# Optimization experiments

Hardware: AMD Instinct MI355X
Metric: run time of the kernel (lower is better)

## Reference

```python
import jax, jax.numpy as jnp
import numpy as np

KSIZE = 3  # median window

def median_blur(x, k):
    # x: [B, C, H, W]; zero padding (k-1)//2, median over k*k window
    # (matches kornia's conv2d-with-binary-kernels + median implementation)
    p = (k - 1) // 2
    xp = jnp.pad(x, ((0, 0), (0, 0), (p, p), (p, p)))
    B, C, H, W = x.shape
    # stack k*k shifted views -> [B, C, H, W, k*k] (k*k=9, small static loop)
    patches = jnp.stack(
        [xp[:, :, i:i + H, j:j + W] for i in range(k) for j in range(k)],
        axis=-1,
    )
    return jnp.median(patches, axis=-1)


def setup_inputs() -> dict:
    key = jax.random.key(0)
    k1, k2, k3 = jax.random.split(key, 3)
    B, C, H, W = 32, 256, 64, 64
    x = jax.random.normal(k1, (B, C, H, W), dtype=jnp.float32)
    # 1x1 conv weight [out_c, in_c] (the trailing 1x1 spatial dims are squeezed)
    conv_w = jax.random.normal(k2, (C, C), dtype=jnp.float32) * (1.0 / np.sqrt(C))
    conv_b = jax.random.normal(k3, (C,), dtype=jnp.float32) * 0.01
    return {"x": x, "conv_w": conv_w, "conv_b": conv_b}


def reference(x, conv_w, conv_b):
    x_denoised = median_blur(x, KSIZE)  # [B, C, H, W]
    # 1x1 conv == per-pixel channel mixing GEMM
    conv_out = jnp.einsum("oc,bchw->bohw", conv_w, x_denoised) + conv_b[None, :, None, None]
    return x + conv_out
```

## Files before the change

kernel.cpp:

```cpp
#include <hip/hip_runtime.h>

typedef float f32x4 __attribute__((ext_vector_type(4)));
typedef __bf16 bf16x8 __attribute__((ext_vector_type(8)));
typedef unsigned short u16x8 __attribute__((ext_vector_type(8)));

__device__ __forceinline__ unsigned short f2bf(float f) {
  union { float f; unsigned u; } v; v.f = f;
  unsigned r = v.u + 0x7FFFu + ((v.u >> 16) & 1u);
  return (unsigned short)(r >> 16);
}

__device__ __forceinline__ float min3f(float a, float b, float c) {
  return fminf(fminf(a, b), c);
}
__device__ __forceinline__ float max3f(float a, float b, float c) {
  return fmaxf(fmaxf(a, b), c);
}
__device__ __forceinline__ float med3f(float a, float b, float c) {
  return __builtin_amdgcn_fmed3f(a, b, c);
}

__device__ __forceinline__ void gload_lds16(const void* g, void* l) {
  __builtin_amdgcn_global_load_lds(
      (const __attribute__((address_space(1))) void*)g,
      (__attribute__((address_space(3))) void*)l, 16, 0, 0);
}

__global__ void wconv_k(const float* __restrict__ w, unsigned short* __restrict__ wbf) {
  int idx  = blockIdx.x * 256 + threadIdx.x;
  int lane = idx & 63;
  int ob   = (idx >> 6) & 15;
  int ks   = idx >> 10;
  int o = (ob << 4) + (lane & 15);
  int c = (ks << 5) + ((lane >> 4) << 3);
  const float* src = w + (o << 8) + c;
  f32x4 v0 = *(const f32x4*)src;
  f32x4 v1 = *(const f32x4*)(src + 4);
  u16x8 ov;
  ov[0] = f2bf(v0[0]); ov[1] = f2bf(v0[1]); ov[2] = f2bf(v0[2]); ov[3] = f2bf(v0[3]);
  ov[4] = f2bf(v1[0]); ov[5] = f2bf(v1[1]); ov[6] = f2bf(v1[2]); ov[7] = f2bf(v1[3]);
  *(u16x8*)(wbf + (idx << 3)) = ov;
}

__launch_bounds__(256, 2)
__global__ void fused_k(const float* __restrict__ x,
                        const unsigned short* __restrict__ wbf,
                        const float* __restrict__ bias,
                        float* __restrict__ out) {
  __shared__ float Xs[128][64];
  __shared__ unsigned short Bt[128][40];

  const int t   = threadIdx.x;
  const int blk = blockIdx.x;
  const int swz = ((blk & 7) << 7) | (blk >> 3);
  const int b   = swz >> 5;
  const int r0  = (swz & 31) << 1;
  const int lane = t & 63;
  const int w    = t >> 6;
  const int g    = lane >> 4;
  const int l15  = lane & 15;

  const int ci  = t >> 3;
  const int s   = t & 7;
  const int px0 = s << 3;
  const int cw  = ci ^ ((s & 3) << 3);
  const bool hasL = (s > 0), hasR = (s < 7);
  const bool zTop = (r0 == 0), zBot = (r0 == 62);

  const float* xb = x + ((size_t)b << 20);

  float bn[4];
  #pragma unroll
  for (int n = 0; n < 4; ++n) bn[n] = bias[(w << 6) + (n << 4) + l15];

  unsigned soff[8];
  #pragma unroll
  for (int p = 0; p < 8; ++p) {
    int cp = (w << 3) + p;
    int gr = r0 + (lane >> 4) - 1;
    gr = gr < 0 ? 0 : (gr > 63 ? 63 : gr);
    int bG = (lane & 15) ^ p;
    soff[p] = ((unsigned)cp << 14) + ((unsigned)gr << 8) + ((unsigned)bG << 4);
  }

  auto stage = [&](int step) {
    const unsigned kso = (unsigned)step << 19;
    #pragma unroll
    for (int p = 0; p < 8; ++p)
      gload_lds16((const char*)xb + (soff[p] + kso), &Xs[(w << 5) + (p << 2)][0]);
  };

  f32x4 acc[8][4];
  #pragma unroll
  for (int m = 0; m < 8; ++m)
    #pragma unroll
    for (int n = 0; n < 4; ++n)
      acc[m][n] = (f32x4){0.f, 0.f, 0.f, 0.f};

  stage(0);
  __syncthreads();

  const int ri0 = ci << 2;
  const int sig = ci & 7;
  const int bA  = ((s << 1)) ^ sig;
  const int bB  = ((s << 1) | 1) ^ sig;

  #pragma unroll
  for (int ks = 0; ks < 8; ++ks) {
    bf16x8 wfc[4];
    #pragma unroll
    for (int n = 0; n < 4; ++n) {
      const int fidx = (((ks << 4) + (w << 2) + n) << 6) + lane;
      wfc[n] = __builtin_bit_cast(bf16x8, *(const u16x8*)(wbf + ((size_t)fidx << 3)));
    }

    f32x4 va[4], vb[4];
    #pragma unroll
    for (int dr = 0; dr < 4; ++dr) {
      const float* rp = &Xs[ri0 + dr][0];
      va[dr] = *(const f32x4*)(rp + (bA << 2));
      vb[dr] = *(const f32x4*)(rp + (bB << 2));
    }
    float le[4], re[4];
    #pragma unroll
    for (int dr = 0; dr < 4; ++dr) {
      le[dr] = __shfl_up(vb[dr][3], 1);
      re[dr] = __shfl_down(va[dr][0], 1);
    }

    if ((ks >> 1) == w) {
      const int h = ks & 1;
      #pragma unroll
      for (int nn = 0; nn < 2; ++nn) {
        const int n  = (h << 1) + nn;
        const int cx = (nn << 4) + l15;
        const int sx = cx & 7;
        const int rb = cx << 2;
        #pragma unroll
        for (int m = 0; m < 8; ++m) {
          const int bL = ((((m & 3) << 2) + g) ^ sx) << 2;
          const f32x4 xv = *(const f32x4*)&Xs[rb + 1 + (m >> 2)][bL];
          acc[m][n] += xv;
        }
      }
    }

    {
      float R0[10], R1[10], R2[10];
      R0[0] = hasL ? le[0] : 0.f; R1[0] = hasL ? le[1] : 0.f; R2[0] = hasL ? le[2] : 0.f;
      R0[9] = hasR ? re[0] : 0.f; R1[9] = hasR ? re[1] : 0.f; R2[9] = hasR ? re[2] : 0.f;
      #pragma unroll
      for (int j = 0; j < 4; ++j) {
        R0[1 + j] = va[0][j]; R0[5 + j] = vb[0][j];
        R1[1 + j] = va[1][j]; R1[5 + j] = vb[1][j];
        R2[1 + j] = va[2][j]; R2[5 + j] = vb[2][j];
      }
      if (zTop) {
        #pragma unroll
        for (int j = 0; j < 10; ++j) R0[j] = 0.f;
      }
      float mn[10], md[10], mx[10];
      #pragma unroll
      for (int j = 0; j < 10; ++j) {
        mn[j] = min3f(R0[j], R1[j], R2[j]);
        md[j] = med3f(R0[j], R1[j], R2[j]);
        mx[j] = max3f(R0[j], R1[j], R2[j]);
      }
      #pragma unroll
      for (int i = 0; i < 8; ++i) {
        float t0 = max3f(mn[i], mn[i+1], mn[i+2]);
        float t1 = med3f(md[i], md[i+1], md[i+2]);
        float t2 = min3f(mx[i], mx[i+1], mx[i+2]);
        Bt[px0 + i][cw] = f2bf(med3f(t0, t1, t2));
      }
    }
    {
      float R0[10], R1[10], R2[10];
      R0[0] = hasL ? le[1] : 0.f; R1[0] = hasL ? le[2] : 0.f; R2[0] = hasL ? le[3] : 0.f;
      R0[9] = hasR ? re[1] : 0.f; R1[9] = hasR ? re[2] : 0.f; R2[9] = hasR ? re[3] : 0.f;
      #pragma unroll
      for (int j = 0; j < 4; ++j) {
        R0[1 + j] = va[1][j]; R0[5 + j] = vb[1][j];
        R1[1 + j] = va[2][j]; R1[5 + j] = vb[2][j];
        R2[1 + j] = va[3][j]; R2[5 + j] = vb[3][j];
      }
      if (zBot) {
        #pragma unroll
        for (int j = 0; j < 10; ++j) R2[j] = 0.f;
      }
      float mn[10], md[10], mx[10];
      #pragma unroll
      for (int j = 0; j < 10; ++j) {
        mn[j] = min3f(R0[j], R1[j], R2[j]);
        md[j] = med3f(R0[j], R1[j], R2[j]);
        mx[j] = max3f(R0[j], R1[j], R2[j]);
      }
      #pragma unroll
      for (int i = 0; i < 8; ++i) {
        float t0 = max3f(mn[i], mn[i+1], mn[i+2]);
        float t1 = med3f(md[i], md[i+1], md[i+2]);
        float t2 = min3f(mx[i], mx[i+1], mx[i+2]);
        Bt[64 + px0 + i][cw] = f2bf(med3f(t0, t1, t2));
      }
    }

    __syncthreads();

    if (ks < 7) stage(ks + 1);

    bf16x8 pa[8];
    #pragma unroll
    for (int m = 0; m < 8; ++m) {
      const int px = (m << 4) + l15;
      const int gc = (g ^ ((px >> 3) & 3)) << 3;
      pa[m] = __builtin_bit_cast(bf16x8, *(const u16x8*)&Bt[px][gc]);
    }
    #pragma unroll
    for (int m = 0; m < 8; ++m)
      #pragma unroll
      for (int n = 0; n < 4; ++n)
        acc[m][n] = __builtin_amdgcn_mfma_f32_16x16x32_bf16(pa[m], wfc[n], acc[m][n], 0, 0, 0);

    if (ks < 7) __syncthreads();
  }

  #pragma unroll
  for (int m = 0; m < 8; ++m) {
    #pragma unroll
    for (int n = 0; n < 4; ++n) {
      const int o = (w << 6) + (n << 4) + l15;
      const size_t idx = ((((size_t)b << 8) + (size_t)o) << 12)
                       + ((size_t)(r0 + (m >> 2)) << 6)
                       + (size_t)(((m & 3) << 4) + (g << 2));
      f32x4 res;
      #pragma unroll
      for (int q = 0; q < 4; ++q) res[q] = acc[m][n][q] + bn[n];
      *(f32x4*)(out + idx) = res;
    }
  }
}

extern "C" void kernel_launch(void* const* d_in, const int* in_sizes, int n_in,
                              void* d_out, int out_size, void* d_ws, size_t ws_size,
                              hipStream_t stream) {
  const float* x  = (const float*)d_in[0];
  const float* cw = (const float*)d_in[1];
  const float* cb = (const float*)d_in[2];
  float* out = (float*)d_out;
  unsigned short* wbf = (unsigned short*)d_ws;

  hipLaunchKernelGGL(wconv_k, dim3(32), dim3(256), 0, stream, cw, wbf);
  hipLaunchKernelGGL(fused_k, dim3(1024), dim3(256), 0, stream, x, wbf, cb, out);
}
```

Baseline: 65.59 us.

## Stage input tile as bf16 in LDS via register prefetch instead of direct LDS loads

The input tile is now loaded into registers, converted to bf16, and written to LDS with a new swizzle, replacing the fp32 direct global-to-LDS loads. This halves LDS footprint and read traffic, and lets the next tile's global loads overlap the MFMA phase. The median and residual now run on bf16-rounded inputs, so the residual term loses precision against the fp32 reference. Output stores also become nontemporal.

```diff
diff --git a/kernel.cpp b/kernel.cpp
--- a/kernel.cpp
+++ b/kernel.cpp
@@ -3,13 +3,28 @@
 typedef float f32x4 __attribute__((ext_vector_type(4)));
 typedef __bf16 bf16x8 __attribute__((ext_vector_type(8)));
 typedef unsigned short u16x8 __attribute__((ext_vector_type(8)));
+typedef unsigned short u16x4 __attribute__((ext_vector_type(4)));
 
 __device__ __forceinline__ unsigned short f2bf(float f) {
   union { float f; unsigned u; } v; v.f = f;
   unsigned r = v.u + 0x7FFFu + ((v.u >> 16) & 1u);
   return (unsigned short)(r >> 16);
 }
-
+__device__ __forceinline__ float bf2f(unsigned short u) {
+  union { unsigned u; float f; } v; v.u = (unsigned)u << 16; return v.f;
+}
+__device__ __forceinline__ unsigned short f2bf_exact(float f) {
+  union { float f; unsigned u; } v; v.f = f;
+  return (unsigned short)(v.u >> 16);
+}
+__device__ __forceinline__ u16x4 cvt4(f32x4 v) {
+  u16x4 o;
+  o[0] = __builtin_bit_cast(unsigned short, (__bf16)v[0]);
+  o[1] = __builtin_bit_cast(unsigned short, (__bf16)v[1]);
+  o[2] = __builtin_bit_cast(unsigned short, (__bf16)v[2]);
+  o[3] = __builtin_bit_cast(unsigned short, (__bf16)v[3]);
+  return o;
+}
 __device__ __forceinline__ float min3f(float a, float b, float c) {
   return fminf(fminf(a, b), c);
 }
@@ -18,12 +33,6 @@
 }
 __device__ __forceinline__ float med3f(float a, float b, float c) {
   return __builtin_amdgcn_fmed3f(a, b, c);
-}
-
-__device__ __forceinline__ void gload_lds16(const void* g, void* l) {
-  __builtin_amdgcn_global_load_lds(
-      (const __attribute__((address_space(1))) void*)g,
-      (__attribute__((address_space(3))) void*)l, 16, 0, 0);
 }
 
 __global__ void wconv_k(const float* __restrict__ w, unsigned short* __restrict__ wbf) {
@@ -47,7 +56,7 @@
                         const unsigned short* __restrict__ wbf,
                         const float* __restrict__ bias,
                         float* __restrict__ out) {
-  __shared__ float Xs[128][64];
+  __shared__ unsigned short Xs[128][64];
   __shared__ unsigned short Bt[128][40];
 
   const int t   = threadIdx.x;
@@ -73,21 +82,31 @@
   #pragma unroll
   for (int n = 0; n < 4; ++n) bn[n] = bias[(w << 6) + (n << 4) + l15];
 
-  unsigned soff[8];
+  const int dr_st = lane >> 4;
+  const int g16   = lane & 15;
+  unsigned soff[8], wdst[8];
   #pragma unroll
   for (int p = 0; p < 8; ++p) {
     int cp = (w << 3) + p;
-    int gr = r0 + (lane >> 4) - 1;
+    int gr = r0 + dr_st - 1;
     gr = gr < 0 ? 0 : (gr > 63 ? 63 : gr);
-    int bG = (lane & 15) ^ p;
-    soff[p] = ((unsigned)cp << 14) + ((unsigned)gr << 8) + ((unsigned)bG << 4);
+    soff[p] = ((unsigned)cp << 14) + ((unsigned)gr << 8) + ((unsigned)g16 << 4);
+    int gs = (g16 >> 1) ^ p ^ dr_st;
+    wdst[p] = (unsigned)(((cp << 2) + dr_st) << 6) + (unsigned)(gs << 3) + (unsigned)((g16 & 1) << 2);
   }
-
-  auto stage = [&](int step) {
+  unsigned short* XsF = &Xs[0][0];
+
+  f32x4 ld[8];
+  auto issue = [&](int step) {
     const unsigned kso = (unsigned)step << 19;
     #pragma unroll
     for (int p = 0; p < 8; ++p)
-      gload_lds16((const char*)xb + (soff[p] + kso), &Xs[(w << 5) + (p << 2)][0]);
+      ld[p] = *(const f32x4*)((const char*)xb + (soff[p] + kso));
+  };
+  auto commit = [&]() {
+    #pragma unroll
+    for (int p = 0; p < 8; ++p)
+      *(u16x4*)&XsF[wdst[p]] = cvt4(ld[p]);
   };
 
   f32x4 acc[8][4];
@@ -97,13 +116,8 @@
     for (int n = 0; n < 4; ++n)
       acc[m][n] = (f32x4){0.f, 0.f, 0.f, 0.f};
 
-  stage(0);
+  issue(0); commit();
   __syncthreads();
-
-  const int ri0 = ci << 2;
-  const int sig = ci & 7;
-  const int bA  = ((s << 1)) ^ sig;
-  const int bB  = ((s << 1) | 1) ^ sig;
 
   #pragma unroll
   for (int ks = 0; ks < 8; ++ks) {
@@ -114,18 +128,11 @@
       wfc[n] = __builtin_bit_cast(bf16x8, *(const u16x8*)(wbf + ((size_t)fidx << 3)));
     }
 
-    f32x4 va[4], vb[4];
+    u16x8 xv[4];
     #pragma unroll
     for (int dr = 0; dr < 4; ++dr) {
-      const float* rp = &Xs[ri0 + dr][0];
-      va[dr] = *(const f32x4*)(rp + (bA << 2));
-      vb[dr] = *(const f32x4*)(rp + (bB << 2));
-    }
-    float le[4], re[4];
-    #pragma unroll
-    for (int dr = 0; dr < 4; ++dr) {
-      le[dr] = __shfl_up(vb[dr][3], 1);
-      re[dr] = __shfl_down(va[dr][0], 1);
+      const int gs = s ^ (ci & 7) ^ dr;
+      xv[dr] = *(const u16x8*)&XsF[(((ci << 2) + dr) << 6) + (gs << 3)];
     }
 
     if ((ks >> 1) == w) {
@@ -134,15 +141,28 @@
       for (int nn = 0; nn < 2; ++nn) {
         const int n  = (h << 1) + nn;
         const int cx = (nn << 4) + l15;
-        const int sx = cx & 7;
-        const int rb = cx << 2;
         #pragma unroll
         for (int m = 0; m < 8; ++m) {
-          const int bL = ((((m & 3) << 2) + g) ^ sx) << 2;
-          const f32x4 xv = *(const f32x4*)&Xs[rb + 1 + (m >> 2)][bL];
-          acc[m][n] += xv;
+          const int dr = 1 + (m >> 2);
+          const int gf = ((m & 3) << 1) + (g >> 1);
+          const int gs = gf ^ (cx & 7) ^ dr;
+          const u16x4 xv4 = *(const u16x4*)&XsF[(((cx << 2) + dr) << 6) + (gs << 3) + ((g & 1) << 2)];
+          #pragma unroll
+          for (int q = 0; q < 4; ++q) acc[m][n][q] += bf2f(xv4[q]);
         }
       }
+    }
+
+    float X[4][8];
+    #pragma unroll
+    for (int dr = 0; dr < 4; ++dr)
+      #pragma unroll
+      for (int j = 0; j < 8; ++j) X[dr][j] = bf2f(xv[dr][j]);
+    float le[4], re[4];
+    #pragma unroll
+    for (int dr = 0; dr < 4; ++dr) {
+      le[dr] = __shfl_up(X[dr][7], 1);
+      re[dr] = __shfl_down(X[dr][0], 1);
     }
 
     {
@@ -150,11 +170,7 @@
       R0[0] = hasL ? le[0] : 0.f; R1[0] = hasL ? le[1] : 0.f; R2[0] = hasL ? le[2] : 0.f;
       R0[9] = hasR ? re[0] : 0.f; R1[9] = hasR ? re[1] : 0.f; R2[9] = hasR ? re[2] : 0.f;
       #pragma unroll
-      for (int j = 0; j < 4; ++j) {
-        R0[1 + j] = va[0][j]; R0[5 + j] = vb[0][j];
-        R1[1 + j] = va[1][j]; R1[5 + j] = vb[1][j];
-        R2[1 + j] = va[2][j]; R2[5 + j] = vb[2][j];
-      }
+      for (int j = 0; j < 8; ++j) { R0[1 + j] = X[0][j]; R1[1 + j] = X[1][j]; R2[1 + j] = X[2][j]; }
       if (zTop) {
         #pragma unroll
         for (int j = 0; j < 10; ++j) R0[j] = 0.f;
@@ -171,7 +187,7 @@
         float t0 = max3f(mn[i], mn[i+1], mn[i+2]);
         float t1 = med3f(md[i], md[i+1], md[i+2]);
         float t2 = min3f(mx[i], mx[i+1], mx[i+2]);
-        Bt[px0 + i][cw] = f2bf(med3f(t0, t1, t2));
+        Bt[px0 + i][cw] = f2bf_exact(med3f(t0, t1, t2));
       }
     }
     {
@@ -179,11 +195,7 @@
       R0[0] = hasL ? le[1] : 0.f; R1[0] = hasL ? le[2] : 0.f; R2[0] = hasL ? le[3] : 0.f;
       R0[9] = hasR ? re[1] : 0.f; R1[9] = hasR ? re[2] : 0.f; R2[9] = hasR ? re[3] : 0.f;
       #pragma unroll
-      for (int j = 0; j < 4; ++j) {
-        R0[1 + j] = va[1][j]; R0[5 + j] = vb[1][j];
-        R1[1 + j] = va[2][j]; R1[5 + j] = vb[2][j];
-        R2[1 + j] = va[3][j]; R2[5 + j] = vb[3][j];
-      }
+      for (int j = 0; j < 8; ++j) { R0[1 + j] = X[1][j]; R1[1 + j] = X[2][j]; R2[1 + j] = X[3][j]; }
       if (zBot) {
         #pragma unroll
         for (int j = 0; j < 10; ++j) R2[j] = 0.f;
@@ -200,13 +212,14 @@
         float t0 = max3f(mn[i], mn[i+1], mn[i+2]);
         float t1 = med3f(md[i], md[i+1], md[i+2]);
         float t2 = min3f(mx[i], mx[i+1], mx[i+2]);
-        Bt[64 + px0 + i][cw] = f2bf(med3f(t0, t1, t2));
+        Bt[64 + px0 + i][cw] = f2bf_exact(med3f(t0, t1, t2));
       }
     }
 
     __syncthreads();
 
-    if (ks < 7) stage(ks + 1);
+    if (ks < 7) issue(ks + 1);
+    __builtin_amdgcn_sched_barrier(0);
 
     bf16x8 pa[8];
     #pragma unroll
@@ -221,7 +234,9 @@
       for (int n = 0; n < 4; ++n)
         acc[m][n] = __builtin_amdgcn_mfma_f32_16x16x32_bf16(pa[m], wfc[n], acc[m][n], 0, 0, 0);
 
-    if (ks < 7) __syncthreads();
+    if (ks < 7) commit();
+
+    __syncthreads();
   }
 
   #pragma unroll
@@ -235,7 +250,7 @@
       f32x4 res;
       #pragma unroll
       for (int q = 0; q < 4; ++q) res[q] = acc[m][n][q] + bn[n];
-      *(f32x4*)(out + idx) = res;
+      __builtin_nontemporal_store(res, (f32x4*)(out + idx));
     }
   }
 }
```

Measured after the change: 97.84 us. 1.49x slower.

## Double-buffer x tiles in LDS with manual waitcnt and barrier scheduling

Applied to the files above, without the earlier changes.

Splits the LDS input tile into two buffers and prefetches the x slab two K-steps ahead, replacing __syncthreads with explicit s_waitcnt/s_barrier and sched_barrier fences. MFMA issue gets raised priority with s_setprio. The residual add moves from per-iteration LDS reads into the epilogue as a global read of x. The aim is to hide global-to-LDS latency behind the median and MFMA work and to drop LDS traffic from the loop. The cost is extra LDS, an extra global read of x, and fragile hand-placed waits: cross-wave visibility and buffer reuse now depend on counter waits rather than full barriers.

```diff
diff --git a/kernel.cpp b/kernel.cpp
--- a/kernel.cpp
+++ b/kernel.cpp
@@ -9,7 +9,6 @@
   unsigned r = v.u + 0x7FFFu + ((v.u >> 16) & 1u);
   return (unsigned short)(r >> 16);
 }
-
 __device__ __forceinline__ float min3f(float a, float b, float c) {
   return fminf(fminf(a, b), c);
 }
@@ -47,7 +46,7 @@
                         const unsigned short* __restrict__ wbf,
                         const float* __restrict__ bias,
                         float* __restrict__ out) {
-  __shared__ float Xs[128][64];
+  __shared__ float Xs[2][128][64];
   __shared__ unsigned short Bt[128][40];
 
   const int t   = threadIdx.x;
@@ -83,11 +82,11 @@
     soff[p] = ((unsigned)cp << 14) + ((unsigned)gr << 8) + ((unsigned)bG << 4);
   }
 
-  auto stage = [&](int step) {
+  auto stage = [&](int step, int buf) {
     const unsigned kso = (unsigned)step << 19;
     #pragma unroll
     for (int p = 0; p < 8; ++p)
-      gload_lds16((const char*)xb + (soff[p] + kso), &Xs[(w << 5) + (p << 2)][0]);
+      gload_lds16((const char*)xb + (soff[p] + kso), &Xs[buf][(w << 5) + (p << 2)][0]);
   };
 
   f32x4 acc[8][4];
@@ -97,8 +96,8 @@
     for (int n = 0; n < 4; ++n)
       acc[m][n] = (f32x4){0.f, 0.f, 0.f, 0.f};
 
-  stage(0);
-  __syncthreads();
+  stage(0, 0);
+  stage(1, 1);
 
   const int ri0 = ci << 2;
   const int sig = ci & 7;
@@ -107,106 +106,98 @@
 
   #pragma unroll
   for (int ks = 0; ks < 8; ++ks) {
+    asm volatile("s_waitcnt vmcnt(8)" ::: "memory");
+    __builtin_amdgcn_sched_barrier(0);
+
+    f32x4 va[4], vb[4];
+    #pragma unroll
+    for (int dr = 0; dr < 4; ++dr) {
+      const float* rp = &Xs[ks & 1][ri0 + dr][0];
+      va[dr] = *(const f32x4*)(rp + (bA << 2));
+      vb[dr] = *(const f32x4*)(rp + (bB << 2));
+    }
+    asm volatile("s_waitcnt lgkmcnt(0)" ::: "memory");
+    __builtin_amdgcn_sched_barrier(0);
+
     bf16x8 wfc[4];
     #pragma unroll
     for (int n = 0; n < 4; ++n) {
       const int fidx = (((ks << 4) + (w << 2) + n) << 6) + lane;
       wfc[n] = __builtin_bit_cast(bf16x8, *(const u16x8*)(wbf + ((size_t)fidx << 3)));
     }
-
-    f32x4 va[4], vb[4];
-    #pragma unroll
-    for (int dr = 0; dr < 4; ++dr) {
-      const float* rp = &Xs[ri0 + dr][0];
-      va[dr] = *(const f32x4*)(rp + (bA << 2));
-      vb[dr] = *(const f32x4*)(rp + (bB << 2));
-    }
-    float le[4], re[4];
-    #pragma unroll
-    for (int dr = 0; dr < 4; ++dr) {
-      le[dr] = __shfl_up(vb[dr][3], 1);
-      re[dr] = __shfl_down(va[dr][0], 1);
-    }
-
-    if ((ks >> 1) == w) {
-      const int h = ks & 1;
+    __builtin_amdgcn_sched_barrier(0);
+    if (ks < 6) stage(ks + 2, ks & 1);
+    __builtin_amdgcn_sched_barrier(0);
+
+    {
+      float le[4], re[4];
       #pragma unroll
-      for (int nn = 0; nn < 2; ++nn) {
-        const int n  = (h << 1) + nn;
-        const int cx = (nn << 4) + l15;
-        const int sx = cx & 7;
-        const int rb = cx << 2;
-        #pragma unroll
-        for (int m = 0; m < 8; ++m) {
-          const int bL = ((((m & 3) << 2) + g) ^ sx) << 2;
-          const f32x4 xv = *(const f32x4*)&Xs[rb + 1 + (m >> 2)][bL];
-          acc[m][n] += xv;
-        }
+      for (int dr = 0; dr < 4; ++dr) {
+        le[dr] = __shfl_up(vb[dr][3], 1);
+        re[dr] = __shfl_down(va[dr][0], 1);
       }
-    }
-
-    {
-      float R0[10], R1[10], R2[10];
-      R0[0] = hasL ? le[0] : 0.f; R1[0] = hasL ? le[1] : 0.f; R2[0] = hasL ? le[2] : 0.f;
-      R0[9] = hasR ? re[0] : 0.f; R1[9] = hasR ? re[1] : 0.f; R2[9] = hasR ? re[2] : 0.f;
-      #pragma unroll
-      for (int j = 0; j < 4; ++j) {
-        R0[1 + j] = va[0][j]; R0[5 + j] = vb[0][j];
-        R1[1 + j] = va[1][j]; R1[5 + j] = vb[1][j];
-        R2[1 + j] = va[2][j]; R2[5 + j] = vb[2][j];
+      {
+        float R0[10], R1[10], R2[10];
+        R0[0] = hasL ? le[0] : 0.f; R1[0] = hasL ? le[1] : 0.f; R2[0] = hasL ? le[2] : 0.f;
+        R0[9] = hasR ? re[0] : 0.f; R1[9] = hasR ? re[1] : 0.f; R2[9] = hasR ? re[2] : 0.f;
+        #pragma unroll
+        for (int j = 0; j < 4; ++j) {
+          R0[1 + j] = va[0][j]; R0[5 + j] = vb[0][j];
+          R1[1 + j] = va[1][j]; R1[5 + j] = vb[1][j];
+          R2[1 + j] = va[2][j]; R2[5 + j] = vb[2][j];
+        }
+        if (zTop) {
+          #pragma unroll
+          for (int j = 0; j < 10; ++j) R0[j] = 0.f;
+        }
+        float mn[10], md[10], mx[10];
+        #pragma unroll
+        for (int j = 0; j < 10; ++j) {
+          mn[j] = min3f(R0[j], R1[j], R2[j]);
+          md[j] = med3f(R0[j], R1[j], R2[j]);
+          mx[j] = max3f(R0[j], R1[j], R2[j]);
+        }
+        #pragma unroll
+        for (int i = 0; i < 8; ++i) {
+          float t0 = max3f(mn[i], mn[i+1], mn[i+2]);
+          float t1 = med3f(md[i], md[i+1], md[i+2]);
+          float t2 = min3f(mx[i], mx[i+1], mx[i+2]);
+          Bt[px0 + i][cw] = f2bf(med3f(t0, t1, t2));
+        }
       }
-      if (zTop) {
-        #pragma unroll
-        for (int j = 0; j < 10; ++j) R0[j] = 0.f;
+      {
+        float R0[10], R1[10], R2[10];
+        R0[0] = hasL ? le[1] : 0.f; R1[0] = hasL ? le[2] : 0.f; R2[0] = hasL ? le[3] : 0.f;
+        R0[9] = hasR ? re[1] : 0.f; R1[9] = hasR ? re[2] : 0.f; R2[9] = hasR ? re[3] : 0.f;
+        #pragma unroll
+        for (int j = 0; j < 4; ++j) {
+          R0[1 + j] = va[1][j]; R0[5 + j] = vb[1][j];
+          R1[1 + j] = va[2][j]; R1[5 + j] = vb[2][j];
+          R2[1 + j] = va[3][j]; R2[5 + j] = vb[3][j];
+        }
+        if (zBot) {
+          #pragma unroll
+          for (int j = 0; j < 10; ++j) R2[j] = 0.f;
+        }
+        float mn[10], md[10], mx[10];
+        #pragma unroll
+        for (int j = 0; j < 10; ++j) {
+          mn[j] = min3f(R0[j], R1[j], R2[j]);
+          md[j] = med3f(R0[j], R1[j], R2[j]);
+          mx[j] = max3f(R0[j], R1[j], R2[j]);
+        }
+        #pragma unroll
+        for (int i = 0; i < 8; ++i) {
+          float t0 = max3f(mn[i], mn[i+1], mn[i+2]);
+          float t1 = med3f(md[i], md[i+1], md[i+2]);
+          float t2 = min3f(mx[i], mx[i+1], mx[i+2]);
+          Bt[64 + px0 + i][cw] = f2bf(med3f(t0, t1, t2));
+        }
       }
-      float mn[10], md[10], mx[10];
-      #pragma unroll
-      for (int j = 0; j < 10; ++j) {
-        mn[j] = min3f(R0[j], R1[j], R2[j]);
-        md[j] = med3f(R0[j], R1[j], R2[j]);
-        mx[j] = max3f(R0[j], R1[j], R2[j]);
-      }
-      #pragma unroll
-      for (int i = 0; i < 8; ++i) {
-        float t0 = max3f(mn[i], mn[i+1], mn[i+2]);
-        float t1 = med3f(md[i], md[i+1], md[i+2]);
-        float t2 = min3f(mx[i], mx[i+1], mx[i+2]);
-        Bt[px0 + i][cw] = f2bf(med3f(t0, t1, t2));
-      }
-    }
-    {
-      float R0[10], R1[10], R2[10];
-      R0[0] = hasL ? le[1] : 0.f; R1[0] = hasL ? le[2] : 0.f; R2[0] = hasL ? le[3] : 0.f;
-      R0[9] = hasR ? re[1] : 0.f; R1[9] = hasR ? re[2] : 0.f; R2[9] = hasR ? re[3] : 0.f;
-      #pragma unroll
-      for (int j = 0; j < 4; ++j) {
-        R0[1 + j] = va[1][j]; R0[5 + j] = vb[1][j];
-        R1[1 + j] = va[2][j]; R1[5 + j] = vb[2][j];
-        R2[1 + j] = va[3][j]; R2[5 + j] = vb[3][j];
-      }
-      if (zBot) {
-        #pragma unroll
-        for (int j = 0; j < 10; ++j) R2[j] = 0.f;
-      }
-      float mn[10], md[10], mx[10];
-      #pragma unroll
-      for (int j = 0; j < 10; ++j) {
-        mn[j] = min3f(R0[j], R1[j], R2[j]);
-        md[j] = med3f(R0[j], R1[j], R2[j]);
-        mx[j] = max3f(R0[j], R1[j], R2[j]);
-      }
-      #pragma unroll
-      for (int i = 0; i < 8; ++i) {
-        float t0 = max3f(mn[i], mn[i+1], mn[i+2]);
-        float t1 = med3f(md[i], md[i+1], md[i+2]);
-        float t2 = min3f(mx[i], mx[i+1], mx[i+2]);
-        Bt[64 + px0 + i][cw] = f2bf(med3f(t0, t1, t2));
-      }
-    }
-
-    __syncthreads();
-
-    if (ks < 7) stage(ks + 1);
+    }
+
+    asm volatile("s_waitcnt lgkmcnt(0)\n\ts_barrier" ::: "memory");
+    __builtin_amdgcn_sched_barrier(0);
 
     bf16x8 pa[8];
     #pragma unroll
@@ -215,13 +206,17 @@
       const int gc = (g ^ ((px >> 3) & 3)) << 3;
       pa[m] = __builtin_bit_cast(bf16x8, *(const u16x8*)&Bt[px][gc]);
     }
+
+    __builtin_amdgcn_s_setprio(1);
     #pragma unroll
     for (int m = 0; m < 8; ++m)
       #pragma unroll
       for (int n = 0; n < 4; ++n)
         acc[m][n] = __builtin_amdgcn_mfma_f32_16x16x32_bf16(pa[m], wfc[n], acc[m][n], 0, 0, 0);
-
-    if (ks < 7) __syncthreads();
+    __builtin_amdgcn_s_setprio(0);
+
+    asm volatile("s_barrier" ::: "memory");
+    __builtin_amdgcn_sched_barrier(0);
   }
 
   #pragma unroll
@@ -232,9 +227,10 @@
       const size_t idx = ((((size_t)b << 8) + (size_t)o) << 12)
                        + ((size_t)(r0 + (m >> 2)) << 6)
                        + (size_t)(((m & 3) << 4) + (g << 2));
+      f32x4 xv = *(const f32x4*)(x + idx);
       f32x4 res;
       #pragma unroll
-      for (int q = 0; q < 4; ++q) res[q] = acc[m][n][q] + bn[n];
+      for (int q = 0; q < 4; ++q) res[q] = xv[q] + acc[m][n][q] + bn[n];
       *(f32x4*)(out + idx) = res;
     }
   }
```

New measurement: 78.56 us. 1.2x slower.

## Double threads per block to 512 and halve per-thread median and MFMA work

Applied to the files above, without the earlier changes.

Launches the fused median+GEMM kernel with 512 threads (8 waves) instead of 256. Each wave now owns 32 output channels instead of 64, and each thread computes medians for 4 pixels instead of 8. Staging, LDS swizzles and residual loads are remapped to match. The goal is lower register pressure and more waves in flight to hide LDS and global latency, at the cost of more shuffles per output and less reuse of each loaded A fragment across MFMAs.

```diff
diff --git a/kernel.cpp b/kernel.cpp
--- a/kernel.cpp
+++ b/kernel.cpp
@@ -42,7 +42,7 @@
   *(u16x8*)(wbf + (idx << 3)) = ov;
 }
 
-__launch_bounds__(256, 2)
+__launch_bounds__(512, 4)
 __global__ void fused_k(const float* __restrict__ x,
                         const unsigned short* __restrict__ wbf,
                         const float* __restrict__ bias,
@@ -60,147 +60,118 @@
   const int g    = lane >> 4;
   const int l15  = lane & 15;
 
-  const int ci  = t >> 3;
-  const int s   = t & 7;
-  const int px0 = s << 3;
-  const int cw  = ci ^ ((s & 3) << 3);
-  const bool hasL = (s > 0), hasR = (s < 7);
+  const int ci  = t >> 4;
+  const int s   = lane & 15;
+  const int px0 = s << 2;
+  const int cw  = ci ^ (((s >> 1) & 3) << 3);
+  const bool hasL = (s > 0), hasR = (s < 15);
   const bool zTop = (r0 == 0), zBot = (r0 == 62);
 
   const float* xb = x + ((size_t)b << 20);
 
-  float bn[4];
-  #pragma unroll
-  for (int n = 0; n < 4; ++n) bn[n] = bias[(w << 6) + (n << 4) + l15];
-
-  unsigned soff[8];
-  #pragma unroll
-  for (int p = 0; p < 8; ++p) {
-    int cp = (w << 3) + p;
+  float bn[2];
+  #pragma unroll
+  for (int n = 0; n < 2; ++n) bn[n] = bias[(w << 5) + (n << 4) + l15];
+
+  unsigned soff[4];
+  #pragma unroll
+  for (int p = 0; p < 4; ++p) {
+    int cp = (w << 2) + p;
     int gr = r0 + (lane >> 4) - 1;
     gr = gr < 0 ? 0 : (gr > 63 ? 63 : gr);
-    int bG = (lane & 15) ^ p;
-    soff[p] = ((unsigned)cp << 14) + ((unsigned)gr << 8) + ((unsigned)bG << 4);
+    int gG = (lane & 15) ^ (cp & 3);
+    soff[p] = ((unsigned)cp << 14) + ((unsigned)gr << 8) + ((unsigned)gG << 4);
   }
 
   auto stage = [&](int step) {
     const unsigned kso = (unsigned)step << 19;
     #pragma unroll
-    for (int p = 0; p < 8; ++p)
-      gload_lds16((const char*)xb + (soff[p] + kso), &Xs[(w << 5) + (p << 2)][0]);
+    for (int p = 0; p < 4; ++p)
+      gload_lds16((const char*)xb + (soff[p] + kso), &Xs[((w << 2) + p) << 2][0]);
   };
 
-  f32x4 acc[8][4];
+  f32x4 acc[8][2];
   #pragma unroll
   for (int m = 0; m < 8; ++m)
     #pragma unroll
-    for (int n = 0; n < 4; ++n)
+    for (int n = 0; n < 2; ++n)
       acc[m][n] = (f32x4){0.f, 0.f, 0.f, 0.f};
 
   stage(0);
   __syncthreads();
 
   const int ri0 = ci << 2;
-  const int sig = ci & 7;
-  const int bA  = ((s << 1)) ^ sig;
-  const int bB  = ((s << 1) | 1) ^ sig;
+  const int gsw = s ^ (ci & 3);
 
   #pragma unroll
   for (int ks = 0; ks < 8; ++ks) {
-    bf16x8 wfc[4];
-    #pragma unroll
-    for (int n = 0; n < 4; ++n) {
-      const int fidx = (((ks << 4) + (w << 2) + n) << 6) + lane;
+    bf16x8 wfc[2];
+    #pragma unroll
+    for (int n = 0; n < 2; ++n) {
+      const int fidx = (((ks << 4) + (w << 1) + n) << 6) + lane;
       wfc[n] = __builtin_bit_cast(bf16x8, *(const u16x8*)(wbf + ((size_t)fidx << 3)));
     }
 
-    f32x4 va[4], vb[4];
+    f32x4 va[4];
+    #pragma unroll
+    for (int dr = 0; dr < 4; ++dr)
+      va[dr] = *(const f32x4*)&Xs[ri0 + dr][gsw << 2];
+    float le[4], re[4];
     #pragma unroll
     for (int dr = 0; dr < 4; ++dr) {
-      const float* rp = &Xs[ri0 + dr][0];
-      va[dr] = *(const f32x4*)(rp + (bA << 2));
-      vb[dr] = *(const f32x4*)(rp + (bB << 2));
-    }
-    float le[4], re[4];
-    #pragma unroll
-    for (int dr = 0; dr < 4; ++dr) {
-      le[dr] = __shfl_up(vb[dr][3], 1);
+      le[dr] = __shfl_up(va[dr][3], 1);
       re[dr] = __shfl_down(va[dr][0], 1);
     }
 
-    if ((ks >> 1) == w) {
-      const int h = ks & 1;
-      #pragma unroll
-      for (int nn = 0; nn < 2; ++nn) {
-        const int n  = (h << 1) + nn;
-        const int cx = (nn << 4) + l15;
-        const int sx = cx & 7;
-        const int rb = cx << 2;
+    if (ks == w) {
+      #pragma unroll
+      for (int n = 0; n < 2; ++n) {
+        const int cx = (n << 4) + l15;
         #pragma unroll
         for (int m = 0; m < 8; ++m) {
-          const int bL = ((((m & 3) << 2) + g) ^ sx) << 2;
-          const f32x4 xv = *(const f32x4*)&Xs[rb + 1 + (m >> 2)][bL];
+          const int dr = 1 + (m >> 2);
+          const int gf = ((m & 3) << 2) + g;
+          const int gs = gf ^ (cx & 3);
+          const f32x4 xv = *(const f32x4*)&Xs[(cx << 2) + dr][gs << 2];
           acc[m][n] += xv;
         }
       }
     }
 
-    {
-      float R0[10], R1[10], R2[10];
-      R0[0] = hasL ? le[0] : 0.f; R1[0] = hasL ? le[1] : 0.f; R2[0] = hasL ? le[2] : 0.f;
-      R0[9] = hasR ? re[0] : 0.f; R1[9] = hasR ? re[1] : 0.f; R2[9] = hasR ? re[2] : 0.f;
+    #pragma unroll
+    for (int strip = 0; strip < 2; ++strip) {
+      const int d0 = strip;
+      float R0[6], R1[6], R2[6];
+      R0[0] = hasL ? le[d0]     : 0.f;  R0[5] = hasR ? re[d0]     : 0.f;
+      R1[0] = hasL ? le[d0 + 1] : 0.f;  R1[5] = hasR ? re[d0 + 1] : 0.f;
+      R2[0] = hasL ? le[d0 + 2] : 0.f;  R2[5] = hasR ? re[d0 + 2] : 0.f;
       #pragma unroll
       for (int j = 0; j < 4; ++j) {
-        R0[1 + j] = va[0][j]; R0[5 + j] = vb[0][j];
-        R1[1 + j] = va[1][j]; R1[5 + j] = vb[1][j];
-        R2[1 + j] = va[2][j]; R2[5 + j] = vb[2][j];
-      }
-      if (zTop) {
+        R0[1 + j] = va[d0][j];
+        R1[1 + j] = va[d0 + 1][j];
+        R2[1 + j] = va[d0 + 2][j];
+      }
+      if (strip == 0 && zTop) {
         #pragma unroll
-        for (int j = 0; j < 10; ++j) R0[j] = 0.f;
-      }
-      float mn[10], md[10], mx[10];
-      #pragma unroll
-      for (int j = 0; j < 10; ++j) {
+        for (int j = 0; j < 6; ++j) R0[j] = 0.f;
+      }
+      if (strip == 1 && zBot) {
+        #pragma unroll
+        for (int j = 0; j < 6; ++j) R2[j] = 0.f;
+      }
+      float mn[6], md[6], mx[6];
+      #pragma unroll
+      for (int j = 0; j < 6; ++j) {
         mn[j] = min3f(R0[j], R1[j], R2[j]);
         md[j] = med3f(R0[j], R1[j], R2[j]);
         mx[j] = max3f(R0[j], R1[j], R2[j]);
       }
       #pragma unroll
-      for (int i = 0; i < 8; ++i) {
+      for (int i = 0; i < 4; ++i) {
         float t0 = max3f(mn[i], mn[i+1], mn[i+2]);
         float t1 = med3f(md[i], md[i+1], md[i+2]);
         float t2 = min3f(mx[i], mx[i+1], mx[i+2]);
-        Bt[px0 + i][cw] = f2bf(med3f(t0, t1, t2));
-      }
-    }
-    {
-      float R0[10], R1[10], R2[10];
-      R0[0] = hasL ? le[1] : 0.f; R1[0] = hasL ? le[2] : 0.f; R2[0] = hasL ? le[3] : 0.f;
-      R0[9] = hasR ? re[1] : 0.f; R1[9] = hasR ? re[2] : 0.f; R2[9] = hasR ? re[3] : 0.f;
-      #pragma unroll
-      for (int j = 0; j < 4; ++j) {
-        R0[1 + j] = va[1][j]; R0[5 + j] = vb[1][j];
-        R1[1 + j] = va[2][j]; R1[5 + j] = vb[2][j];
-        R2[1 + j] = va[3][j]; R2[5 + j] = vb[3][j];
-      }
-      if (zBot) {
-        #pragma unroll
-        for (int j = 0; j < 10; ++j) R2[j] = 0.f;
-      }
-      float mn[10], md[10], mx[10];
-      #pragma unroll
-      for (int j = 0; j < 10; ++j) {
-        mn[j] = min3f(R0[j], R1[j], R2[j]);
-        md[j] = med3f(R0[j], R1[j], R2[j]);
-        mx[j] = max3f(R0[j], R1[j], R2[j]);
-      }
-      #pragma unroll
-      for (int i = 0; i < 8; ++i) {
-        float t0 = max3f(mn[i], mn[i+1], mn[i+2]);
-        float t1 = med3f(md[i], md[i+1], md[i+2]);
-        float t2 = min3f(mx[i], mx[i+1], mx[i+2]);
-        Bt[64 + px0 + i][cw] = f2bf(med3f(t0, t1, t2));
+        Bt[(strip << 6) + px0 + i][cw] = f2bf(med3f(t0, t1, t2));
       }
     }
 
@@ -208,18 +179,15 @@
 
     if (ks < 7) stage(ks + 1);
 
-    bf16x8 pa[8];
     #pragma unroll
     for (int m = 0; m < 8; ++m) {
       const int px = (m << 4) + l15;
       const int gc = (g ^ ((px >> 3) & 3)) << 3;
-      pa[m] = __builtin_bit_cast(bf16x8, *(const u16x8*)&Bt[px][gc]);
-    }
-    #pragma unroll
-    for (int m = 0; m < 8; ++m)
-      #pragma unroll
-      for (int n = 0; n < 4; ++n)
-        acc[m][n] = __builtin_amdgcn_mfma_f32_16x16x32_bf16(pa[m], wfc[n], acc[m][n], 0, 0, 0);
+      bf16x8 pa = __builtin_bit_cast(bf16x8, *(const u16x8*)&Bt[px][gc]);
+      #pragma unroll
+      for (int n = 0; n < 2; ++n)
+        acc[m][n] = __builtin_amdgcn_mfma_f32_16x16x32_bf16(pa, wfc[n], acc[m][n], 0, 0, 0);
+    }
 
     if (ks < 7) __syncthreads();
   }
@@ -227,8 +195,8 @@
   #pragma unroll
   for (int m = 0; m < 8; ++m) {
     #pragma unroll
-    for (int n = 0; n < 4; ++n) {
-      const int o = (w << 6) + (n << 4) + l15;
+    for (int n = 0; n < 2; ++n) {
+      const int o = (w << 5) + (n << 4) + l15;
       const size_t idx = ((((size_t)b << 8) + (size_t)o) << 12)
                        + ((size_t)(r0 + (m >> 2)) << 6)
                        + (size_t)(((m & 3) << 4) + (g << 2));
@@ -250,5 +218,5 @@
   unsigned short* wbf = (unsigned short*)d_ws;
 
   hipLaunchKernelGGL(wconv_k, dim3(32), dim3(256), 0, stream, cw, wbf);
-  hipLaunchKernelGGL(fused_k, dim3(1024), dim3(256), 0, stream, x, wbf, cb, out);
-}
+  hipLaunchKernelGGL(fused_k, dim3(1024), dim3(512), 0, stream, x, wbf, cb, out);
+}
```

Result: slower. 100.7 us (+53.6%).
